# Optimization experiments

Hardware: AMD Instinct MI355X
Metric: run time of the kernel (lower is better)

## Reference

```python
import jax, jax.numpy as jnp
import numpy as np

FORGET_BIAS = 1.0

def _lstm_layer(x_seq, W, b):
    # x_seq: [T, B, D]; W: [D+H, 4H]; b: [4H]
    T, B, _ = x_seq.shape
    H = W.shape[1] // 4
    def step(carry, x):
        c, h = carry
        z = jnp.concatenate([x, h], axis=1) @ W + b  # [B, 4H]
        i, j, f, o = jnp.split(z, 4, axis=1)          # BasicLSTMCell gate order
        new_c = c * jax.nn.sigmoid(f + FORGET_BIAS) + jax.nn.sigmoid(i) * jnp.tanh(j)
        new_h = jnp.tanh(new_c) * jax.nn.sigmoid(o)
        return (new_c, new_h), new_h
    init = (jnp.zeros((B, H), x_seq.dtype), jnp.zeros((B, H), x_seq.dtype))
    _, out = jax.lax.scan(step, init, x_seq)
    return out  # [T, B, H]

def setup_inputs() -> dict:
    key = jax.random.key(0)
    k0, k1, k2 = jax.random.split(key, 3)
    T, B, D, H = 256, 64, 1024, 1024
    scale = 0.05  # keep gates out of saturation
    return {
        "input_seq": jax.random.normal(k0, (T, B, D), dtype=jnp.float32),
        "W0": jax.random.normal(k1, (D + H, 4 * H), dtype=jnp.float32) * scale,
        "b0": jnp.zeros((4 * H,), dtype=jnp.float32),
        "W1": jax.random.normal(k2, (H + H, 4 * H), dtype=jnp.float32) * scale,
        "b1": jnp.zeros((4 * H,), dtype=jnp.float32),
    }

def reference(input_seq, W0, b0, W1, b1):
    # 2-layer static LSTM (training=False -> no dropout)
    h1 = _lstm_layer(input_seq, W0, b0)
    h2 = _lstm_layer(h1, W1, b1)
    return h2
```

## Files before the change

kernel.cpp:

```cpp
#include <hip/hip_runtime.h>
#include <cmath>


typedef _Float16 half8 __attribute__((ext_vector_type(8)));
typedef float f32x4 __attribute__((ext_vector_type(4)));

constexpr int Tt = 256, Bb = 64, Kd = 1024, Gg = 4096;
constexpr int KT = 32;
constexpr size_t MT_ELEMS = (size_t)KT * 64 * 8;

__device__ __forceinline__ f32x4 zero4() { f32x4 z = {0.f, 0.f, 0.f, 0.f}; return z; }
__device__ __forceinline__ float sigmoidf_(float x) { return 1.f / (1.f + expf(-x)); }

__global__ void pack_w_kernel(const float* __restrict__ W0, const float* __restrict__ W1,
                              _Float16* __restrict__ WP0x, _Float16* __restrict__ WP0h,
                              _Float16* __restrict__ WP1x, _Float16* __restrict__ WP1h) {
    int idx = blockIdx.x * 256 + threadIdx.x;
    int half_id = blockIdx.y;
    const float* src = (half_id < 2) ? W0 : W1;
    int rowoff = (half_id & 1) * 1024;
    _Float16* dst = (half_id == 0) ? WP0x : (half_id == 1) ? WP0h : (half_id == 2) ? WP1x : WP1h;

    int lane = idx & 63;
    int kt = (idx >> 6) & 31;
    int nt = idx >> 11;
    int p = nt * 16 + (lane & 15);
    int col = (p & 3) * 1024 + (p >> 2);
    int kbase = rowoff + kt * 32 + (lane >> 4) * 8;
    half8 v;
#pragma unroll
    for (int j = 0; j < 8; ++j) v[j] = (_Float16)src[(size_t)(kbase + j) * Gg + col];
    *reinterpret_cast<half8*>(dst + (size_t)idx * 8) = v;
    (void)kt;
}

__global__ void pack_bias_kernel(const float* __restrict__ b0, const float* __restrict__ b1,
                                 float* __restrict__ bp0, float* __restrict__ bp1) {
    int idx = blockIdx.x * 256 + threadIdx.x;
    int l = idx >> 12, p = idx & 4095;
    int col = (p & 3) * 1024 + (p >> 2);
    (l ? bp1 : bp0)[p] = (l ? b1 : b0)[col];
}

__global__ void pack_a_kernel(const float* __restrict__ X, _Float16* __restrict__ XP) {
    int idx = blockIdx.x * 256 + threadIdx.x;
    int lane = idx & 63;
    int kt = (idx >> 6) & 31;
    int mt = idx >> 11;
    int m = mt * 16 + (lane & 15);
    int kbase = kt * 32 + (lane >> 4) * 8;
    const float* srow = X + (size_t)m * Kd + kbase;
    half8 v;
#pragma unroll
    for (int j = 0; j < 8; ++j) v[j] = (_Float16)srow[j];
    *reinterpret_cast<half8*>(XP + (size_t)idx * 8) = v;
}

__global__ __launch_bounds__(256) void xgemm_kernel(const _Float16* __restrict__ AP,
                                                    const _Float16* __restrict__ WP,
                                                    const float* __restrict__ bias,
                                                    float* __restrict__ Z) {
    int lane = threadIdx.x & 63, wave = threadIdx.x >> 6;
    int wrow = wave >> 1, wcol = wave & 1;
    int mtb = blockIdx.x * 8 + wrow * 4;
    int ntb = blockIdx.y * 8 + wcol * 4;

    f32x4 acc[4][4];
#pragma unroll
    for (int i = 0; i < 4; ++i)
#pragma unroll
        for (int j = 0; j < 4; ++j) acc[i][j] = zero4();

    for (int kt = 0; kt < KT; ++kt) {
        half8 a[4], b[4];
#pragma unroll
        for (int i = 0; i < 4; ++i)
            a[i] = *reinterpret_cast<const half8*>(AP + (((size_t)(mtb + i) * KT + kt) * 64 + lane) * 8);
#pragma unroll
        for (int j = 0; j < 4; ++j)
            b[j] = *reinterpret_cast<const half8*>(WP + (((size_t)(ntb + j) * KT + kt) * 64 + lane) * 8);
#pragma unroll
        for (int i = 0; i < 4; ++i)
#pragma unroll
            for (int j = 0; j < 4; ++j)
                acc[i][j] = __builtin_amdgcn_mfma_f32_16x16x32_f16(a[i], b[j], acc[i][j], 0, 0, 0);
    }

    int r0 = (lane >> 4) * 4, cc = lane & 15;
#pragma unroll
    for (int j = 0; j < 4; ++j) {
        int p = (ntb + j) * 16 + cc;
        float bs = bias[p];
#pragma unroll
        for (int i = 0; i < 4; ++i) {
            int mbase = (mtb + i) * 16 + r0;
#pragma unroll
            for (int r = 0; r < 4; ++r)
                Z[(size_t)(mbase + r) * Gg + p] = acc[i][j][r] + bs;
        }
    }
}

__global__ __launch_bounds__(256) void lstm_step_kernel(const float* __restrict__ ZT,
                                                        const _Float16* __restrict__ hprev,
                                                        const _Float16* __restrict__ WPh,
                                                        float* __restrict__ c,
                                                        _Float16* __restrict__ houtA,
                                                        float* __restrict__ houtF) {
    int lane = threadIdx.x & 63, w = threadIdx.x >> 6;
    int nt = blockIdx.x;

    f32x4 acc = zero4();
    for (int kt = 0; kt < KT; ++kt) {
        half8 a = *reinterpret_cast<const half8*>(hprev + (((size_t)w * KT + kt) * 64 + lane) * 8);
        half8 b = *reinterpret_cast<const half8*>(WPh + (((size_t)nt * KT + kt) * 64 + lane) * 8);
        acc = __builtin_amdgcn_mfma_f32_16x16x32_f16(a, b, acc, 0, 0, 0);
    }

    __shared__ float zs[4][16][17];
    int q = lane >> 4, cc = lane & 15;
#pragma unroll
    for (int r = 0; r < 4; ++r)
        zs[w][q * 4 + r][cc] = acc[r] + ZT[(size_t)(w * 16 + q * 4 + r) * Gg + nt * 16 + cc];
    __syncthreads();

    int bl = lane >> 2, hl = lane & 3;
    float zi = zs[w][bl][hl * 4 + 0];
    float zj = zs[w][bl][hl * 4 + 1];
    float zf = zs[w][bl][hl * 4 + 2];
    float zo = zs[w][bl][hl * 4 + 3];
    int b = w * 16 + bl;
    int hcol = nt * 4 + hl;
    float cold = c[(size_t)b * 1024 + hcol];
    float cn = cold * sigmoidf_(zf + 1.0f) + sigmoidf_(zi) * tanhf(zj);
    float hn = tanhf(cn) * sigmoidf_(zo);
    c[(size_t)b * 1024 + hcol] = cn;
    houtA[(((size_t)w * KT + (hcol >> 5)) * 64 + ((hcol >> 3) & 3) * 16 + bl) * 8 + (hcol & 7)] = (_Float16)hn;
    if (houtF) houtF[(size_t)b * 1024 + hcol] = hn;
}

extern "C" void kernel_launch(void* const* d_in, const int* in_sizes, int n_in,
                              void* d_out, int out_size, void* d_ws, size_t ws_size,
                              hipStream_t stream) {
    const float* X  = (const float*)d_in[0];
    const float* W0 = (const float*)d_in[1];
    const float* b0 = (const float*)d_in[2];
    const float* W1 = (const float*)d_in[3];
    const float* b1 = (const float*)d_in[4];
    float* out = (float*)d_out;

    char* ws = (char*)d_ws;
    size_t off = 0;
    auto take = [&](size_t n) -> void* {
        void* r = ws + off;
        off += (n + 255) & ~(size_t)255;
        return r;
    };

    const size_t WPB = (size_t)Kd * Gg * 2;
    _Float16* WP0x = (_Float16*)take(WPB);
    _Float16* WP0h = (_Float16*)take(WPB);
    _Float16* WP1x = (_Float16*)take(WPB);
    _Float16* WP1h = (_Float16*)take(WPB);
    float* bp0 = (float*)take(Gg * 4);
    float* bp1 = (float*)take(Gg * 4);
    const size_t APB = (size_t)Tt * Bb * Kd * 2;
    _Float16* XP  = (_Float16*)take(APB);
    _Float16* H1P = (_Float16*)take(APB);
    _Float16* hzero = (_Float16*)take((size_t)Bb * 1024 * 2);
    _Float16* h2A   = (_Float16*)take((size_t)2 * Bb * 1024 * 2);
    float* c0 = (float*)take((size_t)Bb * 1024 * 4);
    float* c1 = (float*)take((size_t)Bb * 1024 * 4);

    int Tc = 256;
    while (Tc > 8 && off + (size_t)Tc * Bb * Gg * 4 > ws_size) Tc >>= 1;
    float* Z = (float*)take((size_t)Tc * Bb * Gg * 4);

    hipMemsetAsync(hzero, 0, (size_t)Bb * 1024 * 2, stream);
    hipMemsetAsync(h2A, 0, (size_t)2 * Bb * 1024 * 2, stream);
    hipMemsetAsync(c0, 0, (size_t)Bb * 1024 * 4, stream);
    hipMemsetAsync(c1, 0, (size_t)Bb * 1024 * 4, stream);

    pack_w_kernel<<<dim3(2048, 4), 256, 0, stream>>>(W0, W1, WP0x, WP0h, WP1x, WP1h);
    pack_bias_kernel<<<32, 256, 0, stream>>>(b0, b1, bp0, bp1);
    pack_a_kernel<<<8192, 256, 0, stream>>>(X, XP);

    const size_t hstep = 4 * MT_ELEMS;

    for (int t0 = 0; t0 < Tt; t0 += Tc) {
        xgemm_kernel<<<dim3(Tc * Bb / 128, Gg / 128), 256, 0, stream>>>(
            XP + (size_t)t0 * hstep / 16 * 16, WP0x, bp0, Z);
        for (int t = t0; t < t0 + Tc; ++t) {
            const _Float16* hp = (t == 0) ? hzero : H1P + (size_t)(t - 1) * hstep;
            lstm_step_kernel<<<256, 256, 0, stream>>>(
                Z + (size_t)(t - t0) * Bb * Gg, hp, WP0h, c0,
                H1P + (size_t)t * hstep, nullptr);
        }
    }
    for (int t0 = 0; t0 < Tt; t0 += Tc) {
        xgemm_kernel<<<dim3(Tc * Bb / 128, Gg / 128), 256, 0, stream>>>(
            H1P + (size_t)t0 * hstep, WP1x, bp1, Z);
        for (int t = t0; t < t0 + Tc; ++t) {
            const _Float16* hp = h2A + (size_t)(t & 1) * Bb * 1024;
            _Float16* hw = h2A + (size_t)((t + 1) & 1) * Bb * 1024;
            lstm_step_kernel<<<256, 256, 0, stream>>>(
                Z + (size_t)(t - t0) * Bb * Gg, hp, WP1h, c1,
                hw, out + (size_t)t * Bb * 1024);
        }
    }
    (void)in_sizes; (void)n_in; (void)out_size;
}
```

Measured before the change: 3.364 ms.

## Wavefront-fuse both LSTM layers into one per-step kernel

Both layers now advance in a single launch per step: layer 0 computes step s while layer 1 computes step s-1, each taking half of a 512-block grid. Layer 1 no longer uses a batched input GEMM. It does its full 2048-deep recurrence GEMM inside the step kernel. This halves the number of sequential step launches (257 instead of 512) and drops the second xgemm and the full H1 sequence buffer. The cost is twice the per-step MFMA work for layer-1 blocks and an imbalance between the two halves of the grid.

```diff
diff --git a/kernel.cpp b/kernel.cpp
--- a/kernel.cpp
+++ b/kernel.cpp
@@ -5,33 +5,27 @@
 typedef _Float16 half8 __attribute__((ext_vector_type(8)));
 typedef float f32x4 __attribute__((ext_vector_type(4)));
 
-constexpr int Tt = 256, Bb = 64, Kd = 1024, Gg = 4096;
-constexpr int KT = 32;
-constexpr size_t MT_ELEMS = (size_t)KT * 64 * 8;
+constexpr int Tt = 256, Bb = 64, Gg = 4096;
+constexpr size_t HPACK = 65536;
 
 __device__ __forceinline__ f32x4 zero4() { f32x4 z = {0.f, 0.f, 0.f, 0.f}; return z; }
 __device__ __forceinline__ float sigmoidf_(float x) { return 1.f / (1.f + expf(-x)); }
 
 __global__ void pack_w_kernel(const float* __restrict__ W0, const float* __restrict__ W1,
-                              _Float16* __restrict__ WP0x, _Float16* __restrict__ WP0h,
-                              _Float16* __restrict__ WP1x, _Float16* __restrict__ WP1h) {
+                              _Float16* __restrict__ WP0, _Float16* __restrict__ WP1) {
     int idx = blockIdx.x * 256 + threadIdx.x;
-    int half_id = blockIdx.y;
-    const float* src = (half_id < 2) ? W0 : W1;
-    int rowoff = (half_id & 1) * 1024;
-    _Float16* dst = (half_id == 0) ? WP0x : (half_id == 1) ? WP0h : (half_id == 2) ? WP1x : WP1h;
-
+    const float* src = blockIdx.y ? W1 : W0;
+    _Float16* dst = blockIdx.y ? WP1 : WP0;
     int lane = idx & 63;
-    int kt = (idx >> 6) & 31;
-    int nt = idx >> 11;
+    int kt = (idx >> 6) & 63;
+    int nt = idx >> 12;
     int p = nt * 16 + (lane & 15);
     int col = (p & 3) * 1024 + (p >> 2);
-    int kbase = rowoff + kt * 32 + (lane >> 4) * 8;
+    int kbase = kt * 32 + (lane >> 4) * 8;
     half8 v;
 #pragma unroll
     for (int j = 0; j < 8; ++j) v[j] = (_Float16)src[(size_t)(kbase + j) * Gg + col];
     *reinterpret_cast<half8*>(dst + (size_t)idx * 8) = v;
-    (void)kt;
 }
 
 __global__ void pack_bias_kernel(const float* __restrict__ b0, const float* __restrict__ b1,
@@ -49,7 +43,7 @@
     int mt = idx >> 11;
     int m = mt * 16 + (lane & 15);
     int kbase = kt * 32 + (lane >> 4) * 8;
-    const float* srow = X + (size_t)m * Kd + kbase;
+    const float* srow = X + (size_t)m * 1024 + kbase;
     half8 v;
 #pragma unroll
     for (int j = 0; j < 8; ++j) v[j] = (_Float16)srow[j];
@@ -71,14 +65,14 @@
 #pragma unroll
         for (int j = 0; j < 4; ++j) acc[i][j] = zero4();
 
-    for (int kt = 0; kt < KT; ++kt) {
+    for (int kt = 0; kt < 32; ++kt) {
         half8 a[4], b[4];
 #pragma unroll
         for (int i = 0; i < 4; ++i)
-            a[i] = *reinterpret_cast<const half8*>(AP + (((size_t)(mtb + i) * KT + kt) * 64 + lane) * 8);
+            a[i] = *reinterpret_cast<const half8*>(AP + (((size_t)(mtb + i) * 32 + kt) * 64 + lane) * 8);
 #pragma unroll
         for (int j = 0; j < 4; ++j)
-            b[j] = *reinterpret_cast<const half8*>(WP + (((size_t)(ntb + j) * KT + kt) * 64 + lane) * 8);
+            b[j] = *reinterpret_cast<const half8*>(WP + (((size_t)(ntb + j) * 64 + kt) * 64 + lane) * 8);
 #pragma unroll
         for (int i = 0; i < 4; ++i)
 #pragma unroll
@@ -101,42 +95,82 @@
     }
 }
 
-__global__ __launch_bounds__(256) void lstm_step_kernel(const float* __restrict__ ZT,
-                                                        const _Float16* __restrict__ hprev,
-                                                        const _Float16* __restrict__ WPh,
-                                                        float* __restrict__ c,
-                                                        _Float16* __restrict__ houtA,
-                                                        float* __restrict__ houtF) {
-    int lane = threadIdx.x & 63, w = threadIdx.x >> 6;
-    int nt = blockIdx.x;
-
-    f32x4 acc = zero4();
-    for (int kt = 0; kt < KT; ++kt) {
-        half8 a = *reinterpret_cast<const half8*>(hprev + (((size_t)w * KT + kt) * 64 + lane) * 8);
-        half8 b = *reinterpret_cast<const half8*>(WPh + (((size_t)nt * KT + kt) * 64 + lane) * 8);
-        acc = __builtin_amdgcn_mfma_f32_16x16x32_f16(a, b, acc, 0, 0, 0);
-    }
-
+__global__ __launch_bounds__(256) void lstm_step2_kernel(int s,
+        const float* __restrict__ ZT,
+        const _Float16* __restrict__ WP0,
+        const _Float16* __restrict__ WP1,
+        const float* __restrict__ bp1,
+        const _Float16* __restrict__ h1a,
+        _Float16* __restrict__ h1b,
+        const _Float16* __restrict__ h2a,
+        _Float16* __restrict__ h2b,
+        float* __restrict__ c0, float* __restrict__ c1,
+        float* __restrict__ out) {
+    const int layer = blockIdx.x >> 8;
+    const int nt = blockIdx.x & 255;
+    const int lane = threadIdx.x & 63, w = threadIdx.x >> 6;
     __shared__ float zs[4][16][17];
-    int q = lane >> 4, cc = lane & 15;
-#pragma unroll
-    for (int r = 0; r < 4; ++r)
-        zs[w][q * 4 + r][cc] = acc[r] + ZT[(size_t)(w * 16 + q * 4 + r) * Gg + nt * 16 + cc];
-    __syncthreads();
-
-    int bl = lane >> 2, hl = lane & 3;
-    float zi = zs[w][bl][hl * 4 + 0];
-    float zj = zs[w][bl][hl * 4 + 1];
-    float zf = zs[w][bl][hl * 4 + 2];
-    float zo = zs[w][bl][hl * 4 + 3];
-    int b = w * 16 + bl;
-    int hcol = nt * 4 + hl;
-    float cold = c[(size_t)b * 1024 + hcol];
-    float cn = cold * sigmoidf_(zf + 1.0f) + sigmoidf_(zi) * tanhf(zj);
-    float hn = tanhf(cn) * sigmoidf_(zo);
-    c[(size_t)b * 1024 + hcol] = cn;
-    houtA[(((size_t)w * KT + (hcol >> 5)) * 64 + ((hcol >> 3) & 3) * 16 + bl) * 8 + (hcol & 7)] = (_Float16)hn;
-    if (houtF) houtF[(size_t)b * 1024 + hcol] = hn;
+
+    if (layer == 0) {
+        if (s >= Tt) return;
+        f32x4 acc = zero4();
+        for (int kt = 0; kt < 32; ++kt) {
+            half8 a = *reinterpret_cast<const half8*>(h1a + (((size_t)w * 32 + kt) * 64 + lane) * 8);
+            half8 b = *reinterpret_cast<const half8*>(WP0 + (((size_t)nt * 64 + 32 + kt) * 64 + lane) * 8);
+            acc = __builtin_amdgcn_mfma_f32_16x16x32_f16(a, b, acc, 0, 0, 0);
+        }
+        int q = lane >> 4, cc = lane & 15;
+#pragma unroll
+        for (int r = 0; r < 4; ++r)
+            zs[w][q * 4 + r][cc] = acc[r] + ZT[(size_t)(w * 16 + q * 4 + r) * Gg + nt * 16 + cc];
+        __syncthreads();
+
+        int bl = lane >> 2, hl = lane & 3;
+        float zi = zs[w][bl][hl * 4 + 0];
+        float zj = zs[w][bl][hl * 4 + 1];
+        float zf = zs[w][bl][hl * 4 + 2];
+        float zo = zs[w][bl][hl * 4 + 3];
+        int b = w * 16 + bl;
+        int hcol = nt * 4 + hl;
+        float cold = c0[(size_t)b * 1024 + hcol];
+        float cn = cold * sigmoidf_(zf + 1.0f) + sigmoidf_(zi) * tanhf(zj);
+        float hn = tanhf(cn) * sigmoidf_(zo);
+        c0[(size_t)b * 1024 + hcol] = cn;
+        h1b[(((size_t)w * 32 + (hcol >> 5)) * 64 + ((hcol >> 3) & 3) * 16 + bl) * 8 + (hcol & 7)] = (_Float16)hn;
+    } else {
+        if (s < 1) return;
+        f32x4 acc = zero4();
+        for (int kt = 0; kt < 32; ++kt) {
+            half8 a = *reinterpret_cast<const half8*>(h1a + (((size_t)w * 32 + kt) * 64 + lane) * 8);
+            half8 b = *reinterpret_cast<const half8*>(WP1 + (((size_t)nt * 64 + kt) * 64 + lane) * 8);
+            acc = __builtin_amdgcn_mfma_f32_16x16x32_f16(a, b, acc, 0, 0, 0);
+        }
+        for (int kt = 0; kt < 32; ++kt) {
+            half8 a = *reinterpret_cast<const half8*>(h2a + (((size_t)w * 32 + kt) * 64 + lane) * 8);
+            half8 b = *reinterpret_cast<const half8*>(WP1 + (((size_t)nt * 64 + 32 + kt) * 64 + lane) * 8);
+            acc = __builtin_amdgcn_mfma_f32_16x16x32_f16(a, b, acc, 0, 0, 0);
+        }
+        int q = lane >> 4, cc = lane & 15;
+        float bs = bp1[nt * 16 + cc];
+#pragma unroll
+        for (int r = 0; r < 4; ++r)
+            zs[w][q * 4 + r][cc] = acc[r] + bs;
+        __syncthreads();
+
+        int bl = lane >> 2, hl = lane & 3;
+        float zi = zs[w][bl][hl * 4 + 0];
+        float zj = zs[w][bl][hl * 4 + 1];
+        float zf = zs[w][bl][hl * 4 + 2];
+        float zo = zs[w][bl][hl * 4 + 3];
+        int b = w * 16 + bl;
+        int hcol = nt * 4 + hl;
+        float cold = c1[(size_t)b * 1024 + hcol];
+        float cn = cold * sigmoidf_(zf + 1.0f) + sigmoidf_(zi) * tanhf(zj);
+        float hn = tanhf(cn) * sigmoidf_(zo);
+        c1[(size_t)b * 1024 + hcol] = cn;
+        h2b[(((size_t)w * 32 + (hcol >> 5)) * 64 + ((hcol >> 3) & 3) * 16 + bl) * 8 + (hcol & 7)] = (_Float16)hn;
+        out[(size_t)(s - 1) * 65536 + (size_t)b * 1024 + hcol] = hn;
+    }
 }
 
 extern "C" void kernel_launch(void* const* d_in, const int* in_sizes, int n_in,
@@ -157,18 +191,15 @@
         return r;
     };
 
-    const size_t WPB = (size_t)Kd * Gg * 2;
-    _Float16* WP0x = (_Float16*)take(WPB);
-    _Float16* WP0h = (_Float16*)take(WPB);
-    _Float16* WP1x = (_Float16*)take(WPB);
-    _Float16* WP1h = (_Float16*)take(WPB);
+    const size_t WPB = (size_t)2048 * Gg * 2;
+    _Float16* WP0 = (_Float16*)take(WPB);
+    _Float16* WP1 = (_Float16*)take(WPB);
     float* bp0 = (float*)take(Gg * 4);
     float* bp1 = (float*)take(Gg * 4);
-    const size_t APB = (size_t)Tt * Bb * Kd * 2;
-    _Float16* XP  = (_Float16*)take(APB);
-    _Float16* H1P = (_Float16*)take(APB);
-    _Float16* hzero = (_Float16*)take((size_t)Bb * 1024 * 2);
-    _Float16* h2A   = (_Float16*)take((size_t)2 * Bb * 1024 * 2);
+    const size_t APB = (size_t)Tt * Bb * 1024 * 2;
+    _Float16* XP = (_Float16*)take(APB);
+    _Float16* h1A = (_Float16*)take(2 * HPACK * 2);
+    _Float16* h2A = (_Float16*)take(2 * HPACK * 2);
     float* c0 = (float*)take((size_t)Bb * 1024 * 4);
     float* c1 = (float*)take((size_t)Bb * 1024 * 4);
 
@@ -176,37 +207,31 @@
     while (Tc > 8 && off + (size_t)Tc * Bb * Gg * 4 > ws_size) Tc >>= 1;
     float* Z = (float*)take((size_t)Tc * Bb * Gg * 4);
 
-    hipMemsetAsync(hzero, 0, (size_t)Bb * 1024 * 2, stream);
-    hipMemsetAsync(h2A, 0, (size_t)2 * Bb * 1024 * 2, stream);
+    hipMemsetAsync(h1A, 0, 2 * HPACK * 2, stream);
+    hipMemsetAsync(h2A, 0, 2 * HPACK * 2, stream);
     hipMemsetAsync(c0, 0, (size_t)Bb * 1024 * 4, stream);
     hipMemsetAsync(c1, 0, (size_t)Bb * 1024 * 4, stream);
 
-    pack_w_kernel<<<dim3(2048, 4), 256, 0, stream>>>(W0, W1, WP0x, WP0h, WP1x, WP1h);
+    pack_w_kernel<<<dim3(4096, 2), 256, 0, stream>>>(W0, W1, WP0, WP1);
     pack_bias_kernel<<<32, 256, 0, stream>>>(b0, b1, bp0, bp1);
     pack_a_kernel<<<8192, 256, 0, stream>>>(X, XP);
 
-    const size_t hstep = 4 * MT_ELEMS;
+    auto launch_step = [&](int s, const float* ZT) {
+        const _Float16* h1a = h1A + (size_t)((s + 1) & 1) * HPACK;
+        _Float16* h1b = h1A + (size_t)(s & 1) * HPACK;
+        const _Float16* h2a = h2A + (size_t)(s & 1) * HPACK;
+        _Float16* h2b = h2A + (size_t)((s + 1) & 1) * HPACK;
+        lstm_step2_kernel<<<512, 256, 0, stream>>>(s, ZT, WP0, WP1, bp1,
+                                                   h1a, h1b, h2a, h2b, c0, c1, out);
+    };
 
     for (int t0 = 0; t0 < Tt; t0 += Tc) {
         xgemm_kernel<<<dim3(Tc * Bb / 128, Gg / 128), 256, 0, stream>>>(
-            XP + (size_t)t0 * hstep / 16 * 16, WP0x, bp0, Z);
-        for (int t = t0; t < t0 + Tc; ++t) {
-            const _Float16* hp = (t == 0) ? hzero : H1P + (size_t)(t - 1) * hstep;
-            lstm_step_kernel<<<256, 256, 0, stream>>>(
-                Z + (size_t)(t - t0) * Bb * Gg, hp, WP0h, c0,
-                H1P + (size_t)t * hstep, nullptr);
-        }
-    }
-    for (int t0 = 0; t0 < Tt; t0 += Tc) {
-        xgemm_kernel<<<dim3(Tc * Bb / 128, Gg / 128), 256, 0, stream>>>(
-            H1P + (size_t)t0 * hstep, WP1x, bp1, Z);
-        for (int t = t0; t < t0 + Tc; ++t) {
-            const _Float16* hp = h2A + (size_t)(t & 1) * Bb * 1024;
-            _Float16* hw = h2A + (size_t)((t + 1) & 1) * Bb * 1024;
-            lstm_step_kernel<<<256, 256, 0, stream>>>(
-                Z + (size_t)(t - t0) * Bb * Gg, hp, WP1h, c1,
-                hw, out + (size_t)t * Bb * 1024);
-        }
-    }
-    (void)in_sizes; (void)n_in; (void)out_size;
-}
+            XP + (size_t)t0 * HPACK, WP0, bp0, Z);
+        for (int s = t0; s < t0 + Tc; ++s)
+            launch_step(s, Z + (size_t)(s - t0) * Bb * Gg);
+    }
+    launch_step(Tt, Z);
+
+    (void)in_sizes; (void)n_in; (void)out_size; (void)ws_size;
+}
```

Result: slower. 5.489 ms (+63.2%).
